# Kernel optimization log

Measured on AMD Instinct MI355X. Metric: run time of the kernel, lower is better.

## Reference

```python
import jax, jax.numpy as jnp
import numpy as np

N = 10000
F_IN = 512
HID = 256
C = 16
N_POST_ITER = 4


def setup_inputs() -> dict:
    key = jax.random.key(0)
    ks = jax.random.split(key, 10)
    raw_adj = jax.random.uniform(ks[0], (N, N), dtype=jnp.float32) * 0.01
    A = jax.random.uniform(ks[1], (N, N), dtype=jnp.float32)
    normed_adj = A / jnp.sum(A, axis=1, keepdims=True)  # row-sum-one normalized
    features = jax.random.normal(ks[2], (N, F_IN), dtype=jnp.float32)
    labels = jax.random.randint(ks[3], (N,), 0, C)
    y_onehot = jax.nn.one_hot(labels, C, dtype=jnp.float32)
    train_mask = jax.random.randint(ks[4], (N,), 0, 2).astype(jnp.bool_)
    # GCN belief estimator params (glorot-ish scaling)
    W1 = jax.random.normal(ks[5], (F_IN, HID), dtype=jnp.float32) / np.sqrt(F_IN)
    b1 = jnp.zeros((HID,), dtype=jnp.float32)
    W2 = jax.random.normal(ks[6], (HID, C), dtype=jnp.float32) / np.sqrt(HID)
    b2 = jnp.zeros((C,), dtype=jnp.float32)
    # class-compatibility matrix H (initialized, zero-centered as in init_H)
    H = jax.random.normal(ks[7], (C, C), dtype=jnp.float32) * 0.1
    return {"raw_adj": raw_adj, "normed_adj": normed_adj, "features": features,
            "y_onehot": y_onehot, "train_mask": train_mask,
            "W1": W1, "b1": b1, "W2": W2, "b2": b2, "H": H}


def reference(raw_adj, normed_adj, features, y_onehot, train_mask, W1, b1, W2, b2, H):
    num_class = y_onehot.shape[1]
    # 2-layer GCN belief estimator: adj @ (x @ W) + b
    h = jax.nn.relu(normed_adj @ (features @ W1) + b1)          # [N, HID]
    logits = normed_adj @ (h @ W2) + b2                          # [N, C]
    # post_process: iterative compatibility-guided belief propagation
    prior_belief = jax.nn.softmax(logits, axis=1)
    E_hat = prior_belief - 1.0 / num_class
    B_hat = E_hat
    for _ in range(N_POST_ITER):
        B_hat = E_hat + raw_adj @ (B_hat @ H)
    post_belief = B_hat + 1.0 / num_class
    return post_belief
```

## Files before the change

### kernel.cpp

```cpp
#include <hip/hip_runtime.h>
#include <hip/hip_bf16.h>

#define NN 10000
#define KP 10048
static constexpr float INV_C = 1.0f / 16.0f;

typedef __attribute__((ext_vector_type(8))) short bf16x8;
typedef __attribute__((ext_vector_type(4))) float f32x4;
typedef unsigned short u16;
typedef unsigned int u32;

__device__ __forceinline__ u16 f2b(float f) {
    return __builtin_bit_cast(u16, __float2bfloat16(f));
}
__device__ __forceinline__ float b2f(u16 b) {
    union { u32 u; float f; } v; v.u = ((u32)b) << 16;
    return v.f;
}
__device__ __forceinline__ bf16x8 pack8(f32x4 a, f32x4 b) {
    bf16x8 o;
    o[0]=f2b(a[0]); o[1]=f2b(a[1]); o[2]=f2b(a[2]); o[3]=f2b(a[3]);
    o[4]=f2b(b[0]); o[5]=f2b(b[1]); o[6]=f2b(b[2]); o[7]=f2b(b[3]);
    return o;
}

#define AS1(p) ((__attribute__((address_space(1))) void*)(p))
#define AS3(p) ((__attribute__((address_space(3))) void*)(p))

__global__ __launch_bounds__(256)
void cvt_feat(const float* __restrict__ src, u16* __restrict__ dst)
{
    int c = blockIdx.x * 256 + threadIdx.x;
    size_t base = (size_t)c * 8;
    f32x4 a = *(const f32x4*)(src + base);
    f32x4 b = *(const f32x4*)(src + base + 4);
    *(bf16x8*)(dst + base) = pack8(a, b);
}

__global__ __launch_bounds__(256)
void w12t(const float* __restrict__ W1, const float* __restrict__ W2,
          float* __restrict__ W1T, u16* __restrict__ W2T)
{
    int bid = blockIdx.x, t = threadIdx.x;
    if (bid < 512) {
        int idx = bid * 256 + t;
        int n = idx >> 9, k = idx & 511;
        W1T[idx] = W1[(size_t)k * 256 + n];
    } else {
        int idx = (bid - 512) * 256 + t;
        if (idx < 4096) {
            int n_ = idx >> 8, k_ = idx & 255;
            W2T[idx] = f2b(W2[(size_t)k_ * 16 + n_]);
        }
    }
}

template<int BIAS, int RELU>
__global__ __launch_bounds__(256)
void gemm_a32_bt16(const float* __restrict__ A, int lda, int M, int Ka,
                   const u16* __restrict__ BT, int ldb, int N, int npad,
                   const float* __restrict__ bias,
                   u16* __restrict__ C, int ldc, int K)
{
    __shared__ u16 Asm[64 * 64];
    __shared__ u16 Bsm[256 * 64];
    const int t = threadIdx.x;
    const int lane = t & 63;
    const int w = t >> 6;
    const int row0 = blockIdx.x * 64;
    const int n0 = blockIdx.y * 256;

    const f32x4 fz = {0.f, 0.f, 0.f, 0.f};
    f32x4 acc[4][4];
#pragma unroll
    for (int i = 0; i < 4; ++i)
#pragma unroll
        for (int j = 0; j < 4; ++j) acc[i][j] = fz;

    const int ar = t >> 2, akq = t & 3;
    int agr = row0 + ar; if (agr > M - 1) agr = M - 1;
    const float* asrc = A + (size_t)agr * lda + akq * 16;
    const int aslot0 = (akq * 2) ^ (ar & 7);
    const int aslot1 = (akq * 2 + 1) ^ (ar & 7);
    const int l8 = lane >> 3, sl = lane & 7;

    for (int k0 = 0; k0 < K; k0 += 64) {
        bool aval = (k0 + akq * 16) < Ka;
        f32x4 x0, x1, x2, x3;
        if (aval) {
            x0 = *(const f32x4*)(asrc + k0);
            x1 = *(const f32x4*)(asrc + k0 + 4);
            x2 = *(const f32x4*)(asrc + k0 + 8);
            x3 = *(const f32x4*)(asrc + k0 + 12);
        } else {
            x0 = x1 = x2 = x3 = fz;
        }
#pragma unroll
        for (int i = 0; i < 8; ++i) {
            int lr = i * 32 + w * 8 + l8;
            int gn = n0 + lr; if (gn > N - 1) gn = N - 1;
            int ss = sl ^ (lr & 7);
            const u16* src = BT + (size_t)gn * ldb + k0 + ss * 8;
            __builtin_amdgcn_global_load_lds(AS1(src), AS3(&Bsm[(i * 32 + w * 8) * 64]),
                                             16, 0, 0);
        }
        *(bf16x8*)&Asm[ar * 64 + aslot0 * 8] = pack8(x0, x1);
        *(bf16x8*)&Asm[ar * 64 + aslot1 * 8] = pack8(x2, x3);
        __syncthreads();
#pragma unroll
        for (int kk = 0; kk < 2; ++kk) {
            bf16x8 afr[4], bfr[4];
#pragma unroll
            for (int mi = 0; mi < 4; ++mi) {
                int r = mi * 16 + (lane & 15);
                int s2 = (kk * 4 + (lane >> 4)) ^ (r & 7);
                afr[mi] = *(const bf16x8*)&Asm[r * 64 + s2 * 8];
            }
#pragma unroll
            for (int ni = 0; ni < 4; ++ni) {
                int nr = w * 64 + ni * 16 + (lane & 15);
                int s2 = (kk * 4 + (lane >> 4)) ^ (nr & 7);
                bfr[ni] = *(const bf16x8*)&Bsm[nr * 64 + s2 * 8];
            }
#pragma unroll
            for (int mi = 0; mi < 4; ++mi)
#pragma unroll
                for (int ni = 0; ni < 4; ++ni)
                    acc[mi][ni] = __builtin_amdgcn_mfma_f32_16x16x32_bf16(
                        afr[mi], bfr[ni], acc[mi][ni], 0, 0, 0);
        }
        __syncthreads();
    }
#pragma unroll
    for (int mi = 0; mi < 4; ++mi) {
        int grb = row0 + mi * 16 + (lane >> 4) * 4;
#pragma unroll
        for (int ni = 0; ni < 4; ++ni) {
            int gc = n0 + w * 64 + ni * 16 + (lane & 15);
            if (gc < npad) {
                float bv = (BIAS && gc < N) ? bias[gc] : 0.f;
#pragma unroll
                for (int rg = 0; rg < 4; ++rg) {
                    int gr = grb + rg;
                    if (gr < M) {
                        float v = acc[mi][ni][rg] + bv;
                        if (RELU) v = fmaxf(v, 0.f);
                        C[(size_t)gr * ldc + gc] = f2b(gc < N ? v : 0.f);
                    }
                }
            }
        }
    }
}

template<int CVT>
__global__ __launch_bounds__(256)
void gemm_na(const float* __restrict__ A, const u16* __restrict__ BT,
             u16* __restrict__ Pws, u16* __restrict__ Acvt)
{
    __shared__ u16 Asm[64 * 64];
    __shared__ u16 Bsm[256 * 64];
    const int t = threadIdx.x;
    const int lane = t & 63;
    const int w = t >> 6;
    const int row0 = blockIdx.x * 64;
    const int s = blockIdx.y;
    const int c0 = (157 * s) >> 4, c1 = (157 * (s + 1)) >> 4;

    const f32x4 fz = {0.f, 0.f, 0.f, 0.f};
    f32x4 acc[4][4];
#pragma unroll
    for (int i = 0; i < 4; ++i)
#pragma unroll
        for (int j = 0; j < 4; ++j) acc[i][j] = fz;

    const int ar = t >> 2, akq = t & 3;
    const int grow = row0 + ar;
    const int agr = grow < NN ? grow : NN - 1;
    const float* asrc = A + (size_t)agr * NN + akq * 16;
    const int aslot0 = (akq * 2) ^ (ar & 7);
    const int aslot1 = (akq * 2 + 1) ^ (ar & 7);
    const int l8 = lane >> 3, sl = lane & 7;

    for (int ck = c0; ck < c1; ++ck) {
        const int k0 = ck * 64;
        const int kq0 = k0 + akq * 16;
        bool aval = kq0 < NN;
        f32x4 x0, x1, x2, x3;
        if (aval) {
            x0 = *(const f32x4*)(asrc + k0);
            x1 = *(const f32x4*)(asrc + k0 + 4);
            x2 = *(const f32x4*)(asrc + k0 + 8);
            x3 = *(const f32x4*)(asrc + k0 + 12);
        } else {
            x0 = x1 = x2 = x3 = fz;
        }
#pragma unroll
        for (int i = 0; i < 8; ++i) {
            int lr = i * 32 + w * 8 + l8;
            int ss = sl ^ (lr & 7);
            const u16* src = BT + (size_t)lr * KP + k0 + ss * 8;
            __builtin_amdgcn_global_load_lds(AS1(src), AS3(&Bsm[(i * 32 + w * 8) * 64]),
                                             16, 0, 0);
        }
        bf16x8 p0 = pack8(x0, x1), p1 = pack8(x2, x3);
        *(bf16x8*)&Asm[ar * 64 + aslot0 * 8] = p0;
        *(bf16x8*)&Asm[ar * 64 + aslot1 * 8] = p1;
        if (CVT && grow < NN) {
            *(bf16x8*)(Acvt + (size_t)grow * KP + kq0) = p0;
            *(bf16x8*)(Acvt + (size_t)grow * KP + kq0 + 8) = p1;
        }
        __syncthreads();
#pragma unroll
        for (int kk = 0; kk < 2; ++kk) {
            bf16x8 afr[4], bfr[4];
#pragma unroll
            for (int mi = 0; mi < 4; ++mi) {
                int r = mi * 16 + (lane & 15);
                int s2 = (kk * 4 + (lane >> 4)) ^ (r & 7);
                afr[mi] = *(const bf16x8*)&Asm[r * 64 + s2 * 8];
            }
#pragma unroll
            for (int ni = 0; ni < 4; ++ni) {
                int nr = w * 64 + ni * 16 + (lane & 15);
                int s2 = (kk * 4 + (lane >> 4)) ^ (nr & 7);
                bfr[ni] = *(const bf16x8*)&Bsm[nr * 64 + s2 * 8];
            }
#pragma unroll
            for (int mi = 0; mi < 4; ++mi)
#pragma unroll
                for (int ni = 0; ni < 4; ++ni)
                    acc[mi][ni] = __builtin_amdgcn_mfma_f32_16x16x32_bf16(
                        afr[mi], bfr[ni], acc[mi][ni], 0, 0, 0);
        }
        __syncthreads();
    }
    u16* outp = Pws + (size_t)s * NN * 256;
#pragma unroll
    for (int mi = 0; mi < 4; ++mi) {
        int grb = row0 + mi * 16 + (lane >> 4) * 4;
#pragma unroll
        for (int ni = 0; ni < 4; ++ni) {
            int gc = w * 64 + ni * 16 + (lane & 15);
#pragma unroll
            for (int rg = 0; rg < 4; ++rg) {
                int gr = grb + rg;
                if (gr < NN)
                    outp[(size_t)gr * 256 + gc] = f2b(acc[mi][ni][rg]);
            }
        }
    }
}

__global__ __launch_bounds__(256)
void reduce_h(const u16* __restrict__ Pws, const float* __restrict__ b1,
              u16* __restrict__ hbf)
{
    int i8 = blockIdx.x * 256 + threadIdx.x;
    size_t base = (size_t)i8 * 8;
    int col = (int)(base & 255);
    float v[8];
#pragma unroll
    for (int j = 0; j < 8; ++j) v[j] = b1[col + j];
#pragma unroll
    for (int s = 0; s < 16; ++s) {
        bf16x8 p = *(const bf16x8*)(Pws + (size_t)s * NN * 256 + base);
#pragma unroll
        for (int j = 0; j < 8; ++j) v[j] += b2f((u16)p[j]);
    }
    bf16x8 o;
#pragma unroll
    for (int j = 0; j < 8; ++j) o[j] = f2b(fmaxf(v[j], 0.f));
    *(bf16x8*)(hbf + base) = o;
}

template<int AFP32, int CVT>
__global__ __launch_bounds__(256)
void adj16(const void* __restrict__ Av, long lda,
           const u16* __restrict__ BT,
           float* __restrict__ Pout, int nch, int nchf,
           u16* __restrict__ Acvt)
{
    const int t = threadIdx.x, lane = t & 63, w = t >> 6;
    const int s = blockIdx.y;
    const int rowu = blockIdx.x * 64 + w * 16 + (lane & 15);
    const int row = rowu < NN ? rowu : NN - 1;
    const int kq = (lane >> 4) * 8;
    const u16* brow = BT + (size_t)(lane & 15) * KP + kq;
    const float* a32 = (const float*)Av + (size_t)row * lda + kq;
    const u16*  a16 = (const u16*) Av + (size_t)row * lda + kq;
    u16* cvtp = CVT ? (Acvt + (size_t)rowu * KP + kq) : (u16*)0;
    const bool wok = CVT && (rowu < NN);

    int c0 = (nch * s) >> 3, c1 = (nch * (s + 1)) >> 3;
    int c1f = c1 < nchf ? c1 : nchf;
    f32x4 acc0 = {0.f, 0.f, 0.f, 0.f};
    f32x4 acc1 = {0.f, 0.f, 0.f, 0.f};
    int kc = c0;
    for (; kc + 4 <= c1f; kc += 4) {
        bf16x8 a[4], b[4];
#pragma unroll
        for (int u = 0; u < 4; ++u) {
            if (AFP32) {
                f32x4 x = *(const f32x4*)(a32 + (size_t)(kc + u) * 32);
                f32x4 y = *(const f32x4*)(a32 + (size_t)(kc + u) * 32 + 4);
                a[u] = pack8(x, y);
            } else {
                a[u] = *(const bf16x8*)(a16 + (size_t)(kc + u) * 32);
            }
            b[u] = *(const bf16x8*)(brow + (size_t)(kc + u) * 32);
        }
        if (CVT && wok) {
#pragma unroll
            for (int u = 0; u < 4; ++u)
                *(bf16x8*)(cvtp + (size_t)(kc + u) * 32) = a[u];
        }
        acc0 = __builtin_amdgcn_mfma_f32_16x16x32_bf16(a[0], b[0], acc0, 0, 0, 0);
        acc1 = __builtin_amdgcn_mfma_f32_16x16x32_bf16(a[1], b[1], acc1, 0, 0, 0);
        acc0 = __builtin_amdgcn_mfma_f32_16x16x32_bf16(a[2], b[2], acc0, 0, 0, 0);
        acc1 = __builtin_amdgcn_mfma_f32_16x16x32_bf16(a[3], b[3], acc1, 0, 0, 0);
    }
    for (; kc < c1; ++kc) {
        bf16x8 a = bf16x8{0,0,0,0,0,0,0,0};
        if (AFP32) {
            if (kc * 32 + kq < NN) {
                f32x4 x = *(const f32x4*)(a32 + (size_t)kc * 32);
                f32x4 y = *(const f32x4*)(a32 + (size_t)kc * 32 + 4);
                a = pack8(x, y);
            }
        } else {
            a = *(const bf16x8*)(a16 + (size_t)kc * 32);
        }
        if (CVT && wok)
            *(bf16x8*)(cvtp + (size_t)kc * 32) = a;
        bf16x8 b = *(const bf16x8*)(brow + (size_t)kc * 32);
        acc0 = __builtin_amdgcn_mfma_f32_16x16x32_bf16(a, b, acc0, 0, 0, 0);
    }
    int ob = blockIdx.x * 64 + w * 16 + (lane >> 4) * 4;
#pragma unroll
    for (int rg = 0; rg < 4; ++rg) {
        int orow = ob + rg;
        if (orow < NN)
            Pout[(size_t)s * (NN * 16) + (size_t)orow * 16 + (lane & 15)] =
                acc0[rg] + acc1[rg];
    }
}

__global__ __launch_bounds__(256)
void hw2_mfma(const u16* __restrict__ h, const u16* __restrict__ W2T,
              u16* __restrict__ outT)
{
    const int t = threadIdx.x, lane = t & 63, w = t >> 6;
    int row = blockIdx.x * 64 + w * 16 + (lane & 15);
    int rowc = row < NN ? row : NN - 1;
    const int kq = (lane >> 4) * 8;
    const u16* arow = h + (size_t)rowc * 256 + kq;
    const u16* brow = W2T + (size_t)(lane & 15) * 256 + kq;
    f32x4 acc = {0.f, 0.f, 0.f, 0.f};
#pragma unroll
    for (int kc = 0; kc < 8; ++kc) {
        bf16x8 a = *(const bf16x8*)(arow + kc * 32);
        bf16x8 b = *(const bf16x8*)(brow + kc * 32);
        acc = __builtin_amdgcn_mfma_f32_16x16x32_bf16(a, b, acc, 0, 0, 0);
    }
    int ob = blockIdx.x * 64 + w * 16 + (lane >> 4) * 4;
    int col = lane & 15;
#pragma unroll
    for (int rg = 0; rg < 4; ++rg) {
        int r = ob + rg;
        outT[(size_t)col * KP + r] = f2b(r < NN ? acc[rg] : 0.f);
    }
}

__global__ __launch_bounds__(256)
void softmax_e_h2(const float* __restrict__ P, const float* __restrict__ b2,
                  const float* __restrict__ H, float* __restrict__ E,
                  u16* __restrict__ bhT)
{
    __shared__ float Hs[256];
    const int t = threadIdx.x;
    Hs[t] = H[t];
    __syncthreads();
    const int l = t & 63, w = t >> 6;
    const int g = l >> 2, sub = l & 3;
    const int row = blockIdx.x * 64 + w * 16 + g;
    const bool valid = row < NN;
    float acc[16];
#pragma unroll
    for (int k = 0; k < 16; ++k) acc[k] = 0.f;
    if (valid) {
        const float* p0 = P + (size_t)(sub * 2) * (NN * 16) + (size_t)row * 16;
        const float* p1 = p0 + (size_t)NN * 16;
#pragma unroll
        for (int q = 0; q < 4; ++q) {
            f32x4 a = *(const f32x4*)(p0 + q * 4);
            f32x4 c = *(const f32x4*)(p1 + q * 4);
#pragma unroll
            for (int j = 0; j < 4; ++j) acc[q * 4 + j] = a[j] + c[j];
        }
        if (sub == 0) {
#pragma unroll
            for (int k = 0; k < 16; ++k) acc[k] += b2[k];
        }
    }
#pragma unroll
    for (int m = 1; m <= 2; m <<= 1)
#pragma unroll
        for (int k = 0; k < 16; ++k) acc[k] += __shfl_xor(acc[k], m, 4);
    float e[16];
    if (valid) {
        float mx = acc[0];
#pragma unroll
        for (int k = 1; k < 16; ++k) mx = fmaxf(mx, acc[k]);
        float ssum = 0.f;
#pragma unroll
        for (int k = 0; k < 16; ++k) { e[k] = __expf(acc[k] - mx); ssum += e[k]; }
        float inv = 1.f / ssum;
#pragma unroll
        for (int k = 0; k < 16; ++k) e[k] = e[k] * inv - INV_C;
        f32x4 eq = {e[sub*4+0], e[sub*4+1], e[sub*4+2], e[sub*4+3]};
        *(f32x4*)(E + (size_t)row * 16 + sub * 4) = eq;
    } else {
#pragma unroll
        for (int k = 0; k < 16; ++k) e[k] = 0.f;
    }
    float o[4] = {0.f, 0.f, 0.f, 0.f};
#pragma unroll
    for (int m2 = 0; m2 < 16; ++m2) {
        float x = e[m2];
#pragma unroll
        for (int j = 0; j < 4; ++j) o[j] += x * Hs[m2 * 16 + sub * 4 + j];
    }
#pragma unroll
    for (int j = 0; j < 4; ++j)
        bhT[(size_t)(sub * 4 + j) * KP + row] = f2b(o[j]);
}

template<int LAST>
__global__ __launch_bounds__(256)
void combine_bmm2(const float* __restrict__ E, const float* __restrict__ P,
                  const float* __restrict__ H, u16* __restrict__ bhT,
                  float* __restrict__ out)
{
    __shared__ float Hs[256];
    const int t = threadIdx.x;
    Hs[t] = H[t];
    __syncthreads();
    const int l = t & 63, w = t >> 6;
    const int g = l >> 2, sub = l & 3;
    const int row = blockIdx.x * 64 + w * 16 + g;
    const bool valid = row < NN;
    float acc[16];
#pragma unroll
    for (int k = 0; k < 16; ++k) acc[k] = 0.f;
    if (valid) {
        const float* p0 = P + (size_t)(sub * 2) * (NN * 16) + (size_t)row * 16;
        const float* p1 = p0 + (size_t)NN * 16;
#pragma unroll
        for (int q = 0; q < 4; ++q) {
            f32x4 a = *(const f32x4*)(p0 + q * 4);
            f32x4 c = *(const f32x4*)(p1 + q * 4);
#pragma unroll
            for (int j = 0; j < 4; ++j) acc[q * 4 + j] = a[j] + c[j];
        }
        if (sub == 0) {
            const float* ep = E + (size_t)row * 16;
#pragma unroll
            for (int k = 0; k < 16; ++k) acc[k] += ep[k];
        }
    }
#pragma unroll
    for (int m = 1; m <= 2; m <<= 1)
#pragma unroll
        for (int k = 0; k < 16; ++k) acc[k] += __shfl_xor(acc[k], m, 4);
    if (LAST) {
        if (valid) {
            f32x4 oq = {acc[sub*4+0] + INV_C, acc[sub*4+1] + INV_C,
                        acc[sub*4+2] + INV_C, acc[sub*4+3] + INV_C};
            *(f32x4*)(out + (size_t)row * 16 + sub * 4) = oq;
        }
    } else {
        if (!valid) {
#pragma unroll
            for (int k = 0; k < 16; ++k) acc[k] = 0.f;
        }
        float o[4] = {0.f, 0.f, 0.f, 0.f};
#pragma unroll
        for (int m2 = 0; m2 < 16; ++m2) {
            float x = acc[m2];
#pragma unroll
            for (int j = 0; j < 4; ++j) o[j] += x * Hs[m2 * 16 + sub * 4 + j];
        }
#pragma unroll
        for (int j = 0; j < 4; ++j)
            bhT[(size_t)(sub * 4 + j) * KP + row] = f2b(o[j]);
    }
}

extern "C" void kernel_launch(void* const* d_in, const int* in_sizes, int n_in,
                              void* d_out, int out_size, void* d_ws, size_t ws_size,
                              hipStream_t stream)
{
    const float* raw_adj    = (const float*)d_in[0];
    const float* normed_adj = (const float*)d_in[1];
    const float* features   = (const float*)d_in[2];
    const float* W1 = (const float*)d_in[5];
    const float* b1 = (const float*)d_in[6];
    const float* W2 = (const float*)d_in[7];
    const float* b2 = (const float*)d_in[8];
    const float* H  = (const float*)d_in[9];
    float* out = (float*)d_out;

    char* ws = (char*)d_ws;
    u16*   featbf = (u16*)  (ws + 0);
    float* P      = (float*)(ws + 0);
    float* E      = (float*)(ws + 5120000);
    float* W1T    = (float*)(ws + 10240000);
    u16*   W2T    = (u16*)  (ws + 10764288);
    u16*   XWT    = (u16*)  (ws + 10772480);
    u16*   hbf    = (u16*)  (ws + 15917056);
    u16*   hw2T   = (u16*)  (ws + 21037056);
    u16*   bhT    = (u16*)  (ws + 21358592);
    const bool full = ws_size >= (size_t)304560128;
    const bool mid  = ws_size >= (size_t)222640128;
    const bool low  = ws_size >= (size_t)103600128;
    u16* An_bf = (u16*)(ws + 21680128);
    u16* ArBf  = (u16*)(ws + 21680128);
    u16* Pws   = (u16*)(ws + (full ? 222640128 : 21680128));

    cvt_feat<<<2500, 256, 0, stream>>>(features, featbf);
    w12t<<<528, 256, 0, stream>>>(W1, W2, W1T, W2T);

    gemm_a32_bt16<0, 0><<<dim3(4, 40), 256, 0, stream>>>(
        W1T, 512, 256, 512, featbf, 512, NN, KP, nullptr, XWT, KP, 512);

    if (low) {
        if (full)
            gemm_na<1><<<dim3(157, 16), 256, 0, stream>>>(normed_adj, XWT, Pws, An_bf);
        else
            gemm_na<0><<<dim3(157, 16), 256, 0, stream>>>(normed_adj, XWT, Pws, nullptr);
        reduce_h<<<1250, 256, 0, stream>>>(Pws, b1, hbf);
    } else {
        gemm_a32_bt16<1, 1><<<dim3(157, 1), 256, 0, stream>>>(
            normed_adj, NN, NN, NN, XWT, KP, 256, 256, b1, hbf, 256, KP);
    }

    hw2_mfma<<<157, 256, 0, stream>>>(hbf, W2T, hw2T);

    if (full)
        adj16<0, 0><<<dim3(157, 8), 256, 0, stream>>>(
            (const void*)An_bf, KP, hw2T, P, 314, 314, nullptr);
    else
        adj16<1, 0><<<dim3(157, 8), 256, 0, stream>>>(
            (const void*)normed_adj, NN, hw2T, P, 313, 312, nullptr);

    softmax_e_h2<<<157, 256, 0, stream>>>(P, b2, H, E, bhT);

    for (int it = 0; it < 4; ++it) {
        if (mid) {
            if (it == 0)
                adj16<1, 1><<<dim3(157, 8), 256, 0, stream>>>(
                    (const void*)raw_adj, NN, bhT, P, 314, 312, ArBf);
            else
                adj16<0, 0><<<dim3(157, 8), 256, 0, stream>>>(
                    (const void*)ArBf, KP, bhT, P, 314, 314, nullptr);
        } else {
            adj16<1, 0><<<dim3(157, 8), 256, 0, stream>>>(
                (const void*)raw_adj, NN, bhT, P, 313, 312, nullptr);
        }
        if (it == 3)
            combine_bmm2<1><<<157, 256, 0, stream>>>(E, P, H, nullptr, out);
        else
            combine_bmm2<0><<<157, 256, 0, stream>>>(E, P, H, bhT, nullptr);
    }
}
```

Before: 605.3 us.

## Drop bf16 normed_adj cache and prefetch next A chunk in gemm_na

Removes the path that wrote a bf16 copy of normed_adj during the first adjacency GEMM and reused it for the second adjacency product. The second product now rereads the fp32 normed_adj directly. This trades the extra 200MB bf16 write plus its later read for one 400MB fp32 read. It also software-pipelines gemm_na by loading the next fp32 A chunk into registers after the barrier, overlapping global loads with MFMA compute at the cost of more register pressure.

Measured after the change: 591.9 us (median of 3 runs). 2.2% less time.

```diff
diff --git a/kernel.cpp b/kernel.cpp
--- a/kernel.cpp
+++ b/kernel.cpp
@@ -153,10 +153,9 @@
     }
 }
 
-template<int CVT>
 __global__ __launch_bounds__(256)
 void gemm_na(const float* __restrict__ A, const u16* __restrict__ BT,
-             u16* __restrict__ Pws, u16* __restrict__ Acvt)
+             u16* __restrict__ Pws)
 {
     __shared__ u16 Asm[64 * 64];
     __shared__ u16 Bsm[256 * 64];
@@ -182,12 +181,10 @@
     const int aslot1 = (akq * 2 + 1) ^ (ar & 7);
     const int l8 = lane >> 3, sl = lane & 7;
 
-    for (int ck = c0; ck < c1; ++ck) {
-        const int k0 = ck * 64;
-        const int kq0 = k0 + akq * 16;
-        bool aval = kq0 < NN;
-        f32x4 x0, x1, x2, x3;
-        if (aval) {
+    f32x4 x0, x1, x2, x3;
+    {
+        const int k0 = c0 * 64;
+        if (k0 + akq * 16 < NN) {
             x0 = *(const f32x4*)(asrc + k0);
             x1 = *(const f32x4*)(asrc + k0 + 4);
             x2 = *(const f32x4*)(asrc + k0 + 8);
@@ -195,6 +192,10 @@
         } else {
             x0 = x1 = x2 = x3 = fz;
         }
+    }
+
+    for (int ck = c0; ck < c1; ++ck) {
+        const int k0 = ck * 64;
 #pragma unroll
         for (int i = 0; i < 8; ++i) {
             int lr = i * 32 + w * 8 + l8;
@@ -203,14 +204,20 @@
             __builtin_amdgcn_global_load_lds(AS1(src), AS3(&Bsm[(i * 32 + w * 8) * 64]),
                                              16, 0, 0);
         }
-        bf16x8 p0 = pack8(x0, x1), p1 = pack8(x2, x3);
-        *(bf16x8*)&Asm[ar * 64 + aslot0 * 8] = p0;
-        *(bf16x8*)&Asm[ar * 64 + aslot1 * 8] = p1;
-        if (CVT && grow < NN) {
-            *(bf16x8*)(Acvt + (size_t)grow * KP + kq0) = p0;
-            *(bf16x8*)(Acvt + (size_t)grow * KP + kq0 + 8) = p1;
-        }
+        *(bf16x8*)&Asm[ar * 64 + aslot0 * 8] = pack8(x0, x1);
+        *(bf16x8*)&Asm[ar * 64 + aslot1 * 8] = pack8(x2, x3);
         __syncthreads();
+        {
+            const int kn = k0 + 64;
+            if (ck + 1 < c1 && (kn + akq * 16) < NN) {
+                x0 = *(const f32x4*)(asrc + kn);
+                x1 = *(const f32x4*)(asrc + kn + 4);
+                x2 = *(const f32x4*)(asrc + kn + 8);
+                x3 = *(const f32x4*)(asrc + kn + 12);
+            } else {
+                x0 = x1 = x2 = x3 = fz;
+            }
+        }
 #pragma unroll
         for (int kk = 0; kk < 2; ++kk) {
             bf16x8 afr[4], bfr[4];
@@ -521,12 +528,10 @@
     u16*   hbf    = (u16*)  (ws + 15917056);
     u16*   hw2T   = (u16*)  (ws + 21037056);
     u16*   bhT    = (u16*)  (ws + 21358592);
-    const bool full = ws_size >= (size_t)304560128;
-    const bool mid  = ws_size >= (size_t)222640128;
-    const bool low  = ws_size >= (size_t)103600128;
-    u16* An_bf = (u16*)(ws + 21680128);
-    u16* ArBf  = (u16*)(ws + 21680128);
-    u16* Pws   = (u16*)(ws + (full ? 222640128 : 21680128));
+    const bool mid = ws_size >= (size_t)222640128;
+    const bool low = ws_size >= (size_t)103600128;
+    u16* Pws  = (u16*)(ws + 21680128);
+    u16* ArBf = (u16*)(ws + 21680128);
 
     cvt_feat<<<2500, 256, 0, stream>>>(features, featbf);
     w12t<<<528, 256, 0, stream>>>(W1, W2, W1T, W2T);
@@ -535,10 +540,7 @@
         W1T, 512, 256, 512, featbf, 512, NN, KP, nullptr, XWT, KP, 512);
 
     if (low) {
-        if (full)
-            gemm_na<1><<<dim3(157, 16), 256, 0, stream>>>(normed_adj, XWT, Pws, An_bf);
-        else
-            gemm_na<0><<<dim3(157, 16), 256, 0, stream>>>(normed_adj, XWT, Pws, nullptr);
+        gemm_na<<<dim3(157, 16), 256, 0, stream>>>(normed_adj, XWT, Pws);
         reduce_h<<<1250, 256, 0, stream>>>(Pws, b1, hbf);
     } else {
         gemm_a32_bt16<1, 1><<<dim3(157, 1), 256, 0, stream>>>(
@@ -547,12 +549,8 @@
 
     hw2_mfma<<<157, 256, 0, stream>>>(hbf, W2T, hw2T);
 
-    if (full)
-        adj16<0, 0><<<dim3(157, 8), 256, 0, stream>>>(
-            (const void*)An_bf, KP, hw2T, P, 314, 314, nullptr);
-    else
-        adj16<1, 0><<<dim3(157, 8), 256, 0, stream>>>(
-            (const void*)normed_adj, NN, hw2T, P, 313, 312, nullptr);
+    adj16<1, 0><<<dim3(157, 8), 256, 0, stream>>>(
+        (const void*)normed_adj, NN, hw2T, P, 313, 312, nullptr);
 
     softmax_e_h2<<<157, 256, 0, stream>>>(P, b2, H, E, bhT);
 
```

## Fuse split-K reduction with h@W2, prefetch A in gemm_na, use 13 splits

Applied to the files above, without the earlier changes.

The split-K reduce kernel now also applies ReLU and multiplies by W2 from shared memory, writing the transposed hw2 directly. This removes the separate hw2_mfma kernel, the W2 transpose and the hbf round trip. gemm_na gains a register prefetch of the next A chunk so loads overlap the MFMA work, and the split count drops from 16 to 13, which shrinks the partial-sum workspace and the reduction reads. The workspace thresholds change, and the low-workspace path now reads hbf through reduce_h2 with zero splits. That path appears to sum nothing and would therefore produce wrong results.

Measured after the change: 604.8 us. Within noise of the previous version (-0.1%).

```diff
diff --git a/kernel.cpp b/kernel.cpp
--- a/kernel.cpp
+++ b/kernel.cpp
@@ -38,21 +38,11 @@
 }
 
 __global__ __launch_bounds__(256)
-void w12t(const float* __restrict__ W1, const float* __restrict__ W2,
-          float* __restrict__ W1T, u16* __restrict__ W2T)
-{
-    int bid = blockIdx.x, t = threadIdx.x;
-    if (bid < 512) {
-        int idx = bid * 256 + t;
-        int n = idx >> 9, k = idx & 511;
-        W1T[idx] = W1[(size_t)k * 256 + n];
-    } else {
-        int idx = (bid - 512) * 256 + t;
-        if (idx < 4096) {
-            int n_ = idx >> 8, k_ = idx & 255;
-            W2T[idx] = f2b(W2[(size_t)k_ * 16 + n_]);
-        }
-    }
+void w1t(const float* __restrict__ W1, float* __restrict__ W1T)
+{
+    int idx = blockIdx.x * 256 + threadIdx.x;
+    int n = idx >> 9, k = idx & 511;
+    W1T[idx] = W1[(size_t)k * 256 + n];
 }
 
 template<int BIAS, int RELU>
@@ -165,7 +155,7 @@
     const int w = t >> 6;
     const int row0 = blockIdx.x * 64;
     const int s = blockIdx.y;
-    const int c0 = (157 * s) >> 4, c1 = (157 * (s + 1)) >> 4;
+    const int c0 = (157 * s) / 13, c1 = (157 * (s + 1)) / 13;
 
     const f32x4 fz = {0.f, 0.f, 0.f, 0.f};
     f32x4 acc[4][4];
@@ -182,12 +172,10 @@
     const int aslot1 = (akq * 2 + 1) ^ (ar & 7);
     const int l8 = lane >> 3, sl = lane & 7;
 
-    for (int ck = c0; ck < c1; ++ck) {
-        const int k0 = ck * 64;
-        const int kq0 = k0 + akq * 16;
-        bool aval = kq0 < NN;
-        f32x4 x0, x1, x2, x3;
-        if (aval) {
+    f32x4 x0, x1, x2, x3;
+    {
+        const int k0 = c0 * 64;
+        if (k0 + akq * 16 < NN) {
             x0 = *(const f32x4*)(asrc + k0);
             x1 = *(const f32x4*)(asrc + k0 + 4);
             x2 = *(const f32x4*)(asrc + k0 + 8);
@@ -195,6 +183,11 @@
         } else {
             x0 = x1 = x2 = x3 = fz;
         }
+    }
+
+    for (int ck = c0; ck < c1; ++ck) {
+        const int k0 = ck * 64;
+        const int kq0 = k0 + akq * 16;
 #pragma unroll
         for (int i = 0; i < 8; ++i) {
             int lr = i * 32 + w * 8 + l8;
@@ -211,6 +204,17 @@
             *(bf16x8*)(Acvt + (size_t)grow * KP + kq0 + 8) = p1;
         }
         __syncthreads();
+        {
+            const int kn = k0 + 64;
+            if (ck + 1 < c1 && (kn + akq * 16) < NN) {
+                x0 = *(const f32x4*)(asrc + kn);
+                x1 = *(const f32x4*)(asrc + kn + 4);
+                x2 = *(const f32x4*)(asrc + kn + 8);
+                x3 = *(const f32x4*)(asrc + kn + 12);
+            } else {
+                x0 = x1 = x2 = x3 = fz;
+            }
+        }
 #pragma unroll
         for (int kk = 0; kk < 2; ++kk) {
             bf16x8 afr[4], bfr[4];
@@ -252,26 +256,54 @@
     }
 }
 
-__global__ __launch_bounds__(256)
-void reduce_h(const u16* __restrict__ Pws, const float* __restrict__ b1,
-              u16* __restrict__ hbf)
-{
-    int i8 = blockIdx.x * 256 + threadIdx.x;
-    size_t base = (size_t)i8 * 8;
-    int col = (int)(base & 255);
+template<int NS>
+__global__ __launch_bounds__(256)
+void reduce_h2(const u16* __restrict__ Pws, const float* __restrict__ b1,
+               const float* __restrict__ W2, u16* __restrict__ hw2T)
+{
+    __shared__ float W2s[256 * 16];
+    const int t = threadIdx.x;
+#pragma unroll
+    for (int i = 0; i < 16; ++i) W2s[t + i * 256] = W2[t + i * 256];
+    __syncthreads();
+    if (blockIdx.x == 1250) {
+        if (t < 48 * 16) {
+            int r = NN + (t >> 4), c = t & 15;
+            hw2T[(size_t)c * KP + r] = 0;
+        }
+        return;
+    }
+    const int l = t & 31;
+    const int rg = t >> 5;
+    const int row = blockIdx.x * 8 + rg;
+    const size_t base = (size_t)row * 256 + l * 8;
     float v[8];
 #pragma unroll
-    for (int j = 0; j < 8; ++j) v[j] = b1[col + j];
-#pragma unroll
-    for (int s = 0; s < 16; ++s) {
+    for (int j = 0; j < 8; ++j) v[j] = b1[l * 8 + j];
+#pragma unroll
+    for (int s = 0; s < NS; ++s) {
         bf16x8 p = *(const bf16x8*)(Pws + (size_t)s * NN * 256 + base);
 #pragma unroll
         for (int j = 0; j < 8; ++j) v[j] += b2f((u16)p[j]);
     }
-    bf16x8 o;
-#pragma unroll
-    for (int j = 0; j < 8; ++j) o[j] = f2b(fmaxf(v[j], 0.f));
-    *(bf16x8*)(hbf + base) = o;
+#pragma unroll
+    for (int j = 0; j < 8; ++j) v[j] = fmaxf(v[j], 0.f);
+    float o[16];
+#pragma unroll
+    for (int c = 0; c < 16; ++c) o[c] = 0.f;
+#pragma unroll
+    for (int m = 0; m < 8; ++m) {
+        float x = v[m];
+        const float* wrow = &W2s[(l * 8 + m) * 16];
+#pragma unroll
+        for (int c = 0; c < 16; ++c) o[c] += x * wrow[c];
+    }
+#pragma unroll
+    for (int m = 1; m <= 16; m <<= 1)
+#pragma unroll
+        for (int c = 0; c < 16; ++c) o[c] += __shfl_xor(o[c], m, 32);
+    if (l < 16)
+        hw2T[(size_t)l * KP + row] = f2b(o[l]);
 }
 
 template<int AFP32, int CVT>
@@ -347,32 +379,6 @@
 }
 
 __global__ __launch_bounds__(256)
-void hw2_mfma(const u16* __restrict__ h, const u16* __restrict__ W2T,
-              u16* __restrict__ outT)
-{
-    const int t = threadIdx.x, lane = t & 63, w = t >> 6;
-    int row = blockIdx.x * 64 + w * 16 + (lane & 15);
-    int rowc = row < NN ? row : NN - 1;
-    const int kq = (lane >> 4) * 8;
-    const u16* arow = h + (size_t)rowc * 256 + kq;
-    const u16* brow = W2T + (size_t)(lane & 15) * 256 + kq;
-    f32x4 acc = {0.f, 0.f, 0.f, 0.f};
-#pragma unroll
-    for (int kc = 0; kc < 8; ++kc) {
-        bf16x8 a = *(const bf16x8*)(arow + kc * 32);
-        bf16x8 b = *(const bf16x8*)(brow + kc * 32);
-        acc = __builtin_amdgcn_mfma_f32_16x16x32_bf16(a, b, acc, 0, 0, 0);
-    }
-    int ob = blockIdx.x * 64 + w * 16 + (lane >> 4) * 4;
-    int col = lane & 15;
-#pragma unroll
-    for (int rg = 0; rg < 4; ++rg) {
-        int r = ob + rg;
-        outT[(size_t)col * KP + r] = f2b(r < NN ? acc[rg] : 0.f);
-    }
-}
-
-__global__ __launch_bounds__(256)
 void softmax_e_h2(const float* __restrict__ P, const float* __restrict__ b2,
                   const float* __restrict__ H, float* __restrict__ E,
                   u16* __restrict__ bhT)
@@ -516,36 +522,33 @@
     float* P      = (float*)(ws + 0);
     float* E      = (float*)(ws + 5120000);
     float* W1T    = (float*)(ws + 10240000);
-    u16*   W2T    = (u16*)  (ws + 10764288);
-    u16*   XWT    = (u16*)  (ws + 10772480);
-    u16*   hbf    = (u16*)  (ws + 15917056);
-    u16*   hw2T   = (u16*)  (ws + 21037056);
-    u16*   bhT    = (u16*)  (ws + 21358592);
-    const bool full = ws_size >= (size_t)304560128;
-    const bool mid  = ws_size >= (size_t)222640128;
-    const bool low  = ws_size >= (size_t)103600128;
-    u16* An_bf = (u16*)(ws + 21680128);
-    u16* ArBf  = (u16*)(ws + 21680128);
-    u16* Pws   = (u16*)(ws + (full ? 222640128 : 21680128));
+    u16*   XWT    = (u16*)  (ws + 10764288);
+    u16*   hw2T   = (u16*)  (ws + 15908864);
+    u16*   bhT    = (u16*)  (ws + 16230400);
+    const bool full = ws_size >= (size_t)284071936;
+    const bool low  = ws_size >= (size_t)83111936;
+    u16* An_bf = (u16*)(ws + 16551936);
+    u16* ArBf  = (u16*)(ws + 16551936);
+    u16* Pws   = (u16*)(ws + (full ? 217511936 : 16551936));
 
     cvt_feat<<<2500, 256, 0, stream>>>(features, featbf);
-    w12t<<<528, 256, 0, stream>>>(W1, W2, W1T, W2T);
+    w1t<<<512, 256, 0, stream>>>(W1, W1T);
 
     gemm_a32_bt16<0, 0><<<dim3(4, 40), 256, 0, stream>>>(
         W1T, 512, 256, 512, featbf, 512, NN, KP, nullptr, XWT, KP, 512);
 
     if (low) {
         if (full)
-            gemm_na<1><<<dim3(157, 16), 256, 0, stream>>>(normed_adj, XWT, Pws, An_bf);
+            gemm_na<1><<<dim3(157, 13), 256, 0, stream>>>(normed_adj, XWT, Pws, An_bf);
         else
-            gemm_na<0><<<dim3(157, 16), 256, 0, stream>>>(normed_adj, XWT, Pws, nullptr);
-        reduce_h<<<1250, 256, 0, stream>>>(Pws, b1, hbf);
+            gemm_na<0><<<dim3(157, 13), 256, 0, stream>>>(normed_adj, XWT, Pws, nullptr);
+        reduce_h2<13><<<1251, 256, 0, stream>>>(Pws, b1, W2, hw2T);
     } else {
+        u16* hbf = (u16*)(ws + 0);
         gemm_a32_bt16<1, 1><<<dim3(157, 1), 256, 0, stream>>>(
             normed_adj, NN, NN, NN, XWT, KP, 256, 256, b1, hbf, 256, KP);
-    }
-
-    hw2_mfma<<<157, 256, 0, stream>>>(hbf, W2T, hw2T);
+        reduce_h2<0><<<1251, 256, 0, stream>>>((const u16*)hbf, b1, W2, hw2T);
+    }
 
     if (full)
         adj16<0, 0><<<dim3(157, 8), 256, 0, stream>>>(
@@ -557,7 +560,7 @@
     softmax_e_h2<<<157, 256, 0, stream>>>(P, b2, H, E, bhT);
 
     for (int it = 0; it < 4; ++it) {
-        if (mid) {
+        if (full) {
             if (it == 0)
                 adj16<1, 1><<<dim3(157, 8), 256, 0, stream>>>(
                     (const void*)raw_adj, NN, bhT, P, 314, 312, ArBf);
```
